# Optimization experiments

Measured on AMD Instinct MI355X. Metric: run time of the kernel, lower is better.

The kernel has to match this reference:

```python
import jax, jax.numpy as jnp
import numpy as np

LAMBDA = 0.5
TAU = 1.0
EPS = 1e-8  # torch F.cosine_similarity eps

B, D = 8192, 1024


def setup_inputs() -> dict:
    key = jax.random.key(0)
    k1, k2, k3, k4 = jax.random.split(key, 4)
    return {
        "student_query_emb": jax.random.normal(k1, (B, D), dtype=jnp.float32),
        "student_passage_emb": jax.random.normal(k2, (B, D), dtype=jnp.float32),
        "teacher_query_emb": jax.random.normal(k3, (B, D), dtype=jnp.float32),
        "teacher_passage_emb": jax.random.normal(k4, (B, D), dtype=jnp.float32),
    }


def _mse(a, b):
    d = a - b
    return jnp.mean(d * d)


def _retrieval_loss(q, p):
    # cosine sim = (q . p) / max(||q|| * ||p||, eps); normalize then matmul
    # (avoids the [B,B,D] broadcast intermediate of the torch version)
    qn = q / jnp.maximum(jnp.linalg.norm(q, axis=-1, keepdims=True), EPS)
    pn = p / jnp.maximum(jnp.linalg.norm(p, axis=-1, keepdims=True), EPS)
    logits = jnp.einsum("bd,cd->bc", qn, pn) / TAU  # [B, B]
    # cross-entropy with labels = arange(B): pick the diagonal log-prob
    logprobs = jax.nn.log_softmax(logits, axis=-1)
    return -jnp.mean(jnp.diagonal(logprobs))


def reference(student_query_emb, student_passage_emb, teacher_query_emb, teacher_passage_emb):
    distill = 0.5 * (_mse(student_query_emb, teacher_query_emb)
                     + _mse(student_passage_emb, teacher_passage_emb))
    retrieval = _retrieval_loss(student_query_emb, student_passage_emb)
    return LAMBDA * distill + (1.0 - LAMBDA) * retrieval
```

## Files before the change

### kernel.cpp

```cpp
#include <hip/hip_runtime.h>
#include <hip/hip_bf16.h>

typedef unsigned short u16;
typedef unsigned char u8;
typedef float f32x4 __attribute__((ext_vector_type(4)));
typedef int int4v __attribute__((ext_vector_type(4)));
typedef int int8v __attribute__((ext_vector_type(8)));

#define B_ROWS 8192
#define D_DIM  1024
#define FP8_SCALE 16.0f
#define ACC_UNSCALE (1.0f/256.0f)


__global__ void __launch_bounds__(256) prep_kernel(
    const float* __restrict__ sq, const float* __restrict__ sp,
    const float* __restrict__ tq, const float* __restrict__ tp,
    int* __restrict__ qn, int* __restrict__ pn,
    float* __restrict__ ppq, float* __restrict__ ppp, float* __restrict__ ppd)
{
    const int wave = threadIdx.x >> 6;
    const int l    = threadIdx.x & 63;
    const int r    = blockIdx.x * 4 + wave;
    const size_t rb4 = (size_t)r * (D_DIM / 4);

    const float4* Q4 = (const float4*)sq + rb4;
    const float4* P4 = (const float4*)sp + rb4;
    const float4* A4 = (const float4*)tq + rb4;
    const float4* B4 = (const float4*)tp + rb4;

    float4 qv[4], pv[4];
    float sq2 = 0.f, sp2 = 0.f, dq = 0.f, dp = 0.f, qp = 0.f;
    #pragma unroll
    for (int j = 0; j < 4; ++j) {
        const int idx = j * 64 + l;
        float4 q = Q4[idx], p = P4[idx], a = A4[idx], b = B4[idx];
        qv[j] = q; pv[j] = p;
        sq2 += q.x*q.x + q.y*q.y + q.z*q.z + q.w*q.w;
        sp2 += p.x*p.x + p.y*p.y + p.z*p.z + p.w*p.w;
        float dx = q.x-a.x, dy = q.y-a.y, dz = q.z-a.z, dw = q.w-a.w;
        dq += dx*dx + dy*dy + dz*dz + dw*dw;
        dx = p.x-b.x; dy = p.y-b.y; dz = p.z-b.z; dw = p.w-b.w;
        dp += dx*dx + dy*dy + dz*dz + dw*dw;
        qp += q.x*p.x + q.y*p.y + q.z*p.z + q.w*p.w;
    }

    #pragma unroll
    for (int m = 1; m <= 32; m <<= 1) {
        sq2 += __shfl_xor(sq2, m);
        sp2 += __shfl_xor(sp2, m);
        dq  += __shfl_xor(dq, m);
        dp  += __shfl_xor(dp, m);
        qp  += __shfl_xor(qp, m);
    }

    const float rq = 1.0f / fmaxf(sqrtf(sq2), 1e-8f);
    const float rp = 1.0f / fmaxf(sqrtf(sp2), 1e-8f);

    if (l == 0) {
        ppq[r] = dq;
        ppp[r] = dp;
        ppd[r] = qp * rq * rp;
    }

    const float fq = rq * FP8_SCALE;
    const float fp = rp * FP8_SCALE;
    int* qrow = qn + (size_t)r * (D_DIM / 4);
    int* prow = pn + (size_t)r * (D_DIM / 4);
    #pragma unroll
    for (int j = 0; j < 4; ++j) {
        const int idx = j * 64 + l;
        int pk = __builtin_amdgcn_cvt_pk_fp8_f32(qv[j].x * fq, qv[j].y * fq, 0, false);
        pk     = __builtin_amdgcn_cvt_pk_fp8_f32(qv[j].z * fq, qv[j].w * fq, pk, true);
        qrow[idx] = pk;
        pk = __builtin_amdgcn_cvt_pk_fp8_f32(pv[j].x * fp, pv[j].y * fp, 0, false);
        pk = __builtin_amdgcn_cvt_pk_fp8_f32(pv[j].z * fp, pv[j].w * fp, pk, true);
        prow[idx] = pk;
    }
}

__global__ void __launch_bounds__(256) gemm_rowsum_kernel(
    const u8* __restrict__ Q, const u8* __restrict__ P,
    float* __restrict__ gpart)
{
    __shared__ u8 smA[128 * 128];
    __shared__ u8 smB[128 * 128];

    const int tid  = threadIdx.x;
    const int wave = tid >> 6;
    const int lane = tid & 63;
    const int bm = blockIdx.y;
    const int bn = blockIdx.x;

    const int lrow   = lane >> 3;
    const int gchunk = (lane & 7) ^ lrow;
    const u8* Ag = Q + ((size_t)bm * 128) * D_DIM + gchunk * 16;
    const u8* Bg = P + ((size_t)bn * 128) * D_DIM + gchunk * 16;

    const int quad  = lane >> 4;
    const int rw    = lane & 15;
    const int r7    = lane & 7;
    const int arow0 = (wave >> 1) * 64;
    const int bcol0 = (wave & 1) * 64;

    const int off_lo = ((2 * quad) ^ r7) * 16;
    const int off_hi = ((2 * quad + 1) ^ r7) * 16;

    f32x4 acc[4][4];
    #pragma unroll
    for (int i = 0; i < 4; ++i)
        #pragma unroll
        for (int j = 0; j < 4; ++j)
            acc[i][j] = (f32x4){0.f, 0.f, 0.f, 0.f};

    for (int k0 = 0; k0 < D_DIM; k0 += 128) {
        #pragma unroll
        for (int i = 0; i < 4; ++i) {
            const int r0 = wave * 32 + i * 8;
            __builtin_amdgcn_global_load_lds(
                (const __attribute__((address_space(1))) void*)(Ag + (size_t)(r0 + lrow) * D_DIM + k0),
                (__attribute__((address_space(3))) void*)(smA + r0 * 128), 16, 0, 0);
            __builtin_amdgcn_global_load_lds(
                (const __attribute__((address_space(1))) void*)(Bg + (size_t)(r0 + lrow) * D_DIM + k0),
                (__attribute__((address_space(3))) void*)(smB + r0 * 128), 16, 0, 0);
        }
        __syncthreads();

        union Frag { int8v v8; struct { int4v lo, hi; } h; };
        Frag af[4], bf[4];
        #pragma unroll
        for (int mi = 0; mi < 4; ++mi)
            af[mi].h.lo = *(const int4v*)(smA + (arow0 + mi * 16 + rw) * 128 + off_lo);
        #pragma unroll
        for (int ni = 0; ni < 4; ++ni)
            bf[ni].h.lo = *(const int4v*)(smB + (bcol0 + ni * 16 + rw) * 128 + off_lo);
        __builtin_amdgcn_sched_barrier(0);
        #pragma unroll
        for (int mi = 0; mi < 4; ++mi)
            af[mi].h.hi = *(const int4v*)(smA + (arow0 + mi * 16 + rw) * 128 + off_hi);
        #pragma unroll
        for (int ni = 0; ni < 4; ++ni)
            bf[ni].h.hi = *(const int4v*)(smB + (bcol0 + ni * 16 + rw) * 128 + off_hi);

        #pragma unroll
        for (int mi = 0; mi < 4; ++mi)
            #pragma unroll
            for (int ni = 0; ni < 4; ++ni)
                acc[mi][ni] = __builtin_amdgcn_mfma_scale_f32_16x16x128_f8f6f4(
                    af[mi].v8, bf[ni].v8, acc[mi][ni],
                    0, 0,
                    0, 0x7f7f7f7f,
                    0, 0x7f7f7f7f);
        __syncthreads();
    }

    float esum[4][4];
    #pragma unroll
    for (int mi = 0; mi < 4; ++mi)
        #pragma unroll
        for (int r = 0; r < 4; ++r) {
            float s = 0.f;
            #pragma unroll
            for (int ni = 0; ni < 4; ++ni)
                s += __expf(acc[mi][ni][r] * ACC_UNSCALE);
            esum[mi][r] = s;
        }
    #pragma unroll
    for (int m = 1; m <= 8; m <<= 1)
        #pragma unroll
        for (int mi = 0; mi < 4; ++mi)
            #pragma unroll
            for (int r = 0; r < 4; ++r)
                esum[mi][r] += __shfl_xor(esum[mi][r], m);

    if (rw == 0) {
        float* dst = gpart + ((size_t)(bn * 2 + (wave & 1))) * B_ROWS
                   + bm * 128 + arow0;
        #pragma unroll
        for (int mi = 0; mi < 4; ++mi)
            #pragma unroll
            for (int r = 0; r < 4; ++r)
                dst[mi * 16 + quad * 4 + r] = esum[mi][r];
    }
}

__global__ void __launch_bounds__(256) reduce_kernel(
    const float* __restrict__ gpart,
    const float* __restrict__ ppq, const float* __restrict__ ppp,
    const float* __restrict__ ppd, float4* __restrict__ bpart)
{
    const int t = threadIdx.x;
    const int r = blockIdx.x * 256 + t;
    float s = 0.f;
    #pragma unroll 8
    for (int j = 0; j < 128; ++j) s += gpart[(size_t)j * B_ROWS + r];
    float ls = logf(s);
    float v2 = ppq[r], v3 = ppp[r], v4 = ppd[r];
    #pragma unroll
    for (int m = 1; m <= 32; m <<= 1) {
        ls += __shfl_xor(ls, m);
        v2 += __shfl_xor(v2, m);
        v3 += __shfl_xor(v3, m);
        v4 += __shfl_xor(v4, m);
    }
    __shared__ float red[4][4];
    if ((t & 63) == 0) {
        red[t >> 6][0] = ls; red[t >> 6][1] = v2;
        red[t >> 6][2] = v3; red[t >> 6][3] = v4;
    }
    __syncthreads();
    if (t == 0) {
        float4 o;
        o.x = red[0][0] + red[1][0] + red[2][0] + red[3][0];
        o.y = red[0][1] + red[1][1] + red[2][1] + red[3][1];
        o.z = red[0][2] + red[1][2] + red[2][2] + red[3][2];
        o.w = red[0][3] + red[1][3] + red[2][3] + red[3][3];
        bpart[blockIdx.x] = o;
    }
}

__global__ void __launch_bounds__(64) finalize_kernel(
    const float4* __restrict__ bpart, float* __restrict__ out)
{
    const int t = threadIdx.x;
    float4 v = (t < 32) ? bpart[t] : (float4){0.f, 0.f, 0.f, 0.f};
    #pragma unroll
    for (int m = 1; m <= 16; m <<= 1) {
        v.x += __shfl_xor(v.x, m);
        v.y += __shfl_xor(v.y, m);
        v.z += __shfl_xor(v.z, m);
        v.w += __shfl_xor(v.w, m);
    }
    if (t == 0) {
        const float inv_bd = 1.0f / ((float)B_ROWS * (float)D_DIM);
        float distill   = 0.5f * (v.y + v.z) * inv_bd;
        float retrieval = (v.x - v.w) / (float)B_ROWS;
        out[0] = 0.5f * distill + 0.5f * retrieval;
    }
}

extern "C" void kernel_launch(void* const* d_in, const int* in_sizes, int n_in,
                              void* d_out, int out_size, void* d_ws, size_t ws_size,
                              hipStream_t stream) {
    const float* sq = (const float*)d_in[0];
    const float* sp = (const float*)d_in[1];
    const float* tq = (const float*)d_in[2];
    const float* tp = (const float*)d_in[3];

    char* ws = (char*)d_ws;
    float*  ppq   = (float*)(ws);
    float*  ppp   = (float*)(ws + 32768);
    float*  ppd   = (float*)(ws + 65536);
    float4* bpart = (float4*)(ws + 98304);
    float*  gpart = (float*)(ws + 131072);
    int*    qn    = (int*)(ws + 131072 + (size_t)128 * B_ROWS * 4);
    int*    pn    = (int*)((char*)qn + (size_t)B_ROWS * D_DIM);

    prep_kernel<<<B_ROWS / 4, 256, 0, stream>>>(sq, sp, tq, tp, qn, pn, ppq, ppp, ppd);
    gemm_rowsum_kernel<<<dim3(64, 64), 256, 0, stream>>>((const u8*)qn, (const u8*)pn, gpart);
    reduce_kernel<<<32, 256, 0, stream>>>(gpart, ppq, ppp, ppd, bpart);
    finalize_kernel<<<1, 64, 0, stream>>>(bpart, (float*)d_out);
}
```

Before: 244.1 us.

## Use two waves per 128x128 tile with 64x128 per-wave subtiles

The GEMM block shrinks from four waves to two, and each wave now computes a 64x128 output subtile (4x8 MFMA accumulators) instead of 64x64. This raises register-level reuse of the A fragments and halves the per-row partial sums written to gpart, so the reduce kernel reads 64 partials instead of 128. The cost is doubled accumulator registers per wave and fewer waves per block to hide LDS and global load latency. B fragments are loaded per column tile, interleaved with the MFMAs.

Measured after the change: 252.2 us. 3.3% more time.

```diff
diff --git a/kernel.cpp b/kernel.cpp
--- a/kernel.cpp
+++ b/kernel.cpp
@@ -79,7 +79,7 @@
     }
 }
 
-__global__ void __launch_bounds__(256) gemm_rowsum_kernel(
+__global__ void __launch_bounds__(128, 2) gemm_rowsum_kernel(
     const u8* __restrict__ Q, const u8* __restrict__ P,
     float* __restrict__ gpart)
 {
@@ -100,23 +100,24 @@
     const int quad  = lane >> 4;
     const int rw    = lane & 15;
     const int r7    = lane & 7;
-    const int arow0 = (wave >> 1) * 64;
-    const int bcol0 = (wave & 1) * 64;
+    const int arow0 = wave * 64;
 
     const int off_lo = ((2 * quad) ^ r7) * 16;
     const int off_hi = ((2 * quad + 1) ^ r7) * 16;
 
-    f32x4 acc[4][4];
+    f32x4 acc[4][8];
     #pragma unroll
     for (int i = 0; i < 4; ++i)
         #pragma unroll
-        for (int j = 0; j < 4; ++j)
+        for (int j = 0; j < 8; ++j)
             acc[i][j] = (f32x4){0.f, 0.f, 0.f, 0.f};
 
+    union Frag { int8v v8; struct { int4v lo, hi; } h; };
+
     for (int k0 = 0; k0 < D_DIM; k0 += 128) {
         #pragma unroll
-        for (int i = 0; i < 4; ++i) {
-            const int r0 = wave * 32 + i * 8;
+        for (int i = 0; i < 8; ++i) {
+            const int r0 = wave * 64 + i * 8;
             __builtin_amdgcn_global_load_lds(
                 (const __attribute__((address_space(1))) void*)(Ag + (size_t)(r0 + lrow) * D_DIM + k0),
                 (__attribute__((address_space(3))) void*)(smA + r0 * 128), 16, 0, 0);
@@ -126,31 +127,27 @@
         }
         __syncthreads();
 
-        union Frag { int8v v8; struct { int4v lo, hi; } h; };
-        Frag af[4], bf[4];
-        #pragma unroll
-        for (int mi = 0; mi < 4; ++mi)
-            af[mi].h.lo = *(const int4v*)(smA + (arow0 + mi * 16 + rw) * 128 + off_lo);
-        #pragma unroll
-        for (int ni = 0; ni < 4; ++ni)
-            bf[ni].h.lo = *(const int4v*)(smB + (bcol0 + ni * 16 + rw) * 128 + off_lo);
-        __builtin_amdgcn_sched_barrier(0);
-        #pragma unroll
-        for (int mi = 0; mi < 4; ++mi)
-            af[mi].h.hi = *(const int4v*)(smA + (arow0 + mi * 16 + rw) * 128 + off_hi);
-        #pragma unroll
-        for (int ni = 0; ni < 4; ++ni)
-            bf[ni].h.hi = *(const int4v*)(smB + (bcol0 + ni * 16 + rw) * 128 + off_hi);
-
-        #pragma unroll
-        for (int mi = 0; mi < 4; ++mi)
-            #pragma unroll
-            for (int ni = 0; ni < 4; ++ni)
+        Frag af[4];
+        #pragma unroll
+        for (int mi = 0; mi < 4; ++mi) {
+            const u8* row = smA + (arow0 + mi * 16 + rw) * 128;
+            af[mi].h.lo = *(const int4v*)(row + off_lo);
+            af[mi].h.hi = *(const int4v*)(row + off_hi);
+        }
+        #pragma unroll
+        for (int ni = 0; ni < 8; ++ni) {
+            Frag bf;
+            const u8* row = smB + (ni * 16 + rw) * 128;
+            bf.h.lo = *(const int4v*)(row + off_lo);
+            bf.h.hi = *(const int4v*)(row + off_hi);
+            #pragma unroll
+            for (int mi = 0; mi < 4; ++mi)
                 acc[mi][ni] = __builtin_amdgcn_mfma_scale_f32_16x16x128_f8f6f4(
-                    af[mi].v8, bf[ni].v8, acc[mi][ni],
+                    af[mi].v8, bf.v8, acc[mi][ni],
                     0, 0,
                     0, 0x7f7f7f7f,
                     0, 0x7f7f7f7f);
+        }
         __syncthreads();
     }
 
@@ -161,7 +158,7 @@
         for (int r = 0; r < 4; ++r) {
             float s = 0.f;
             #pragma unroll
-            for (int ni = 0; ni < 4; ++ni)
+            for (int ni = 0; ni < 8; ++ni)
                 s += __expf(acc[mi][ni][r] * ACC_UNSCALE);
             esum[mi][r] = s;
         }
@@ -174,8 +171,7 @@
                 esum[mi][r] += __shfl_xor(esum[mi][r], m);
 
     if (rw == 0) {
-        float* dst = gpart + ((size_t)(bn * 2 + (wave & 1))) * B_ROWS
-                   + bm * 128 + arow0;
+        float* dst = gpart + (size_t)bn * B_ROWS + bm * 128 + arow0;
         #pragma unroll
         for (int mi = 0; mi < 4; ++mi)
             #pragma unroll
@@ -193,7 +189,7 @@
     const int r = blockIdx.x * 256 + t;
     float s = 0.f;
     #pragma unroll 8
-    for (int j = 0; j < 128; ++j) s += gpart[(size_t)j * B_ROWS + r];
+    for (int j = 0; j < 64; ++j) s += gpart[(size_t)j * B_ROWS + r];
     float ls = logf(s);
     float v2 = ppq[r], v3 = ppp[r], v4 = ppd[r];
     #pragma unroll
@@ -253,11 +249,11 @@
     float*  ppd   = (float*)(ws + 65536);
     float4* bpart = (float4*)(ws + 98304);
     float*  gpart = (float*)(ws + 131072);
-    int*    qn    = (int*)(ws + 131072 + (size_t)128 * B_ROWS * 4);
+    int*    qn    = (int*)(ws + 131072 + (size_t)64 * B_ROWS * 4);
     int*    pn    = (int*)((char*)qn + (size_t)B_ROWS * D_DIM);
 
     prep_kernel<<<B_ROWS / 4, 256, 0, stream>>>(sq, sp, tq, tp, qn, pn, ppq, ppp, ppd);
-    gemm_rowsum_kernel<<<dim3(64, 64), 256, 0, stream>>>((const u8*)qn, (const u8*)pn, gpart);
+    gemm_rowsum_kernel<<<dim3(64, 64), 128, 0, stream>>>((const u8*)qn, (const u8*)pn, gpart);
     reduce_kernel<<<32, 256, 0, stream>>>(gpart, ppq, ppp, ppd, bpart);
     finalize_kernel<<<1, 64, 0, stream>>>(bpart, (float*)d_out);
 }
```

## Fuse prep, GEMM, reduce and finalize into one persistent kernel with grid barriers

Applied to the files above, without the earlier changes.

Replaces the four separate launches with a single persistent kernel of 512 blocks. The blocks step through the prep rows, GEMM tiles and reductions in turn, separated by atomic-counter grid barriers, and the counters are reset with a memset before launch. The aim is to remove the launch gaps and tail effects between stages. In exchange, every block must be co-resident for the barriers to make progress, the GEMM loses the scheduling of a large hardware grid, and an extra memset call is added.

New measurement: 641.3 us. 163% more time.

```diff
diff --git a/kernel.cpp b/kernel.cpp
--- a/kernel.cpp
+++ b/kernel.cpp
@@ -1,7 +1,6 @@
 #include <hip/hip_runtime.h>
 #include <hip/hip_bf16.h>
 
-typedef unsigned short u16;
 typedef unsigned char u8;
 typedef float f32x4 __attribute__((ext_vector_type(4)));
 typedef int int4v __attribute__((ext_vector_type(4)));
@@ -11,231 +10,239 @@
 #define D_DIM  1024
 #define FP8_SCALE 16.0f
 #define ACC_UNSCALE (1.0f/256.0f)
-
-
-__global__ void __launch_bounds__(256) prep_kernel(
+#define NBLK 512
+
+
+__device__ __forceinline__ void grid_barrier(int* ctr) {
+    __syncthreads();
+    if (threadIdx.x == 0) {
+        __threadfence();
+        __hip_atomic_fetch_add(ctr, 1, __ATOMIC_ACQ_REL, __HIP_MEMORY_SCOPE_AGENT);
+        while (__hip_atomic_load(ctr, __ATOMIC_ACQUIRE, __HIP_MEMORY_SCOPE_AGENT) < NBLK)
+            __builtin_amdgcn_s_sleep(2);
+        __threadfence();
+    }
+    __syncthreads();
+}
+
+__global__ void __launch_bounds__(256, 4) mega_kernel(
     const float* __restrict__ sq, const float* __restrict__ sp,
     const float* __restrict__ tq, const float* __restrict__ tp,
     int* __restrict__ qn, int* __restrict__ pn,
-    float* __restrict__ ppq, float* __restrict__ ppp, float* __restrict__ ppd)
-{
-    const int wave = threadIdx.x >> 6;
-    const int l    = threadIdx.x & 63;
-    const int r    = blockIdx.x * 4 + wave;
-    const size_t rb4 = (size_t)r * (D_DIM / 4);
-
-    const float4* Q4 = (const float4*)sq + rb4;
-    const float4* P4 = (const float4*)sp + rb4;
-    const float4* A4 = (const float4*)tq + rb4;
-    const float4* B4 = (const float4*)tp + rb4;
-
-    float4 qv[4], pv[4];
-    float sq2 = 0.f, sp2 = 0.f, dq = 0.f, dp = 0.f, qp = 0.f;
-    #pragma unroll
-    for (int j = 0; j < 4; ++j) {
-        const int idx = j * 64 + l;
-        float4 q = Q4[idx], p = P4[idx], a = A4[idx], b = B4[idx];
-        qv[j] = q; pv[j] = p;
-        sq2 += q.x*q.x + q.y*q.y + q.z*q.z + q.w*q.w;
-        sp2 += p.x*p.x + p.y*p.y + p.z*p.z + p.w*p.w;
-        float dx = q.x-a.x, dy = q.y-a.y, dz = q.z-a.z, dw = q.w-a.w;
-        dq += dx*dx + dy*dy + dz*dz + dw*dw;
-        dx = p.x-b.x; dy = p.y-b.y; dz = p.z-b.z; dw = p.w-b.w;
-        dp += dx*dx + dy*dy + dz*dz + dw*dw;
-        qp += q.x*p.x + q.y*p.y + q.z*p.z + q.w*p.w;
-    }
-
-    #pragma unroll
-    for (int m = 1; m <= 32; m <<= 1) {
-        sq2 += __shfl_xor(sq2, m);
-        sp2 += __shfl_xor(sp2, m);
-        dq  += __shfl_xor(dq, m);
-        dp  += __shfl_xor(dp, m);
-        qp  += __shfl_xor(qp, m);
-    }
-
-    const float rq = 1.0f / fmaxf(sqrtf(sq2), 1e-8f);
-    const float rp = 1.0f / fmaxf(sqrtf(sp2), 1e-8f);
-
-    if (l == 0) {
-        ppq[r] = dq;
-        ppp[r] = dp;
-        ppd[r] = qp * rq * rp;
-    }
-
-    const float fq = rq * FP8_SCALE;
-    const float fp = rp * FP8_SCALE;
-    int* qrow = qn + (size_t)r * (D_DIM / 4);
-    int* prow = pn + (size_t)r * (D_DIM / 4);
-    #pragma unroll
-    for (int j = 0; j < 4; ++j) {
-        const int idx = j * 64 + l;
-        int pk = __builtin_amdgcn_cvt_pk_fp8_f32(qv[j].x * fq, qv[j].y * fq, 0, false);
-        pk     = __builtin_amdgcn_cvt_pk_fp8_f32(qv[j].z * fq, qv[j].w * fq, pk, true);
-        qrow[idx] = pk;
-        pk = __builtin_amdgcn_cvt_pk_fp8_f32(pv[j].x * fp, pv[j].y * fp, 0, false);
-        pk = __builtin_amdgcn_cvt_pk_fp8_f32(pv[j].z * fp, pv[j].w * fp, pk, true);
-        prow[idx] = pk;
-    }
-}
-
-__global__ void __launch_bounds__(256) gemm_rowsum_kernel(
-    const u8* __restrict__ Q, const u8* __restrict__ P,
-    float* __restrict__ gpart)
+    float* __restrict__ ppq, float* __restrict__ ppp, float* __restrict__ ppd,
+    float* __restrict__ gpart, float4* __restrict__ bpart,
+    int* __restrict__ ctrs, float* __restrict__ out)
 {
     __shared__ u8 smA[128 * 128];
     __shared__ u8 smB[128 * 128];
+    __shared__ float red[4][4];
 
     const int tid  = threadIdx.x;
     const int wave = tid >> 6;
     const int lane = tid & 63;
-    const int bm = blockIdx.y;
-    const int bn = blockIdx.x;
-
-    const int lrow   = lane >> 3;
-    const int gchunk = (lane & 7) ^ lrow;
-    const u8* Ag = Q + ((size_t)bm * 128) * D_DIM + gchunk * 16;
-    const u8* Bg = P + ((size_t)bn * 128) * D_DIM + gchunk * 16;
-
-    const int quad  = lane >> 4;
-    const int rw    = lane & 15;
-    const int r7    = lane & 7;
-    const int arow0 = (wave >> 1) * 64;
-    const int bcol0 = (wave & 1) * 64;
-
-    const int off_lo = ((2 * quad) ^ r7) * 16;
-    const int off_hi = ((2 * quad + 1) ^ r7) * 16;
-
-    f32x4 acc[4][4];
-    #pragma unroll
-    for (int i = 0; i < 4; ++i)
-        #pragma unroll
-        for (int j = 0; j < 4; ++j)
-            acc[i][j] = (f32x4){0.f, 0.f, 0.f, 0.f};
-
-    for (int k0 = 0; k0 < D_DIM; k0 += 128) {
-        #pragma unroll
-        for (int i = 0; i < 4; ++i) {
-            const int r0 = wave * 32 + i * 8;
-            __builtin_amdgcn_global_load_lds(
-                (const __attribute__((address_space(1))) void*)(Ag + (size_t)(r0 + lrow) * D_DIM + k0),
-                (__attribute__((address_space(3))) void*)(smA + r0 * 128), 16, 0, 0);
-            __builtin_amdgcn_global_load_lds(
-                (const __attribute__((address_space(1))) void*)(Bg + (size_t)(r0 + lrow) * D_DIM + k0),
-                (__attribute__((address_space(3))) void*)(smB + r0 * 128), 16, 0, 0);
+    const int b    = blockIdx.x;
+
+    #pragma unroll 1
+    for (int i = 0; i < 4; ++i) {
+        const int r = b * 4 + wave + i * 2048;
+        const size_t rb4 = (size_t)r * (D_DIM / 4);
+        const float4* Q4 = (const float4*)sq + rb4;
+        const float4* P4 = (const float4*)sp + rb4;
+        const float4* A4 = (const float4*)tq + rb4;
+        const float4* B4 = (const float4*)tp + rb4;
+
+        float4 qv[4], pv[4];
+        float sq2 = 0.f, sp2 = 0.f, dq = 0.f, dp = 0.f, qp = 0.f;
+        #pragma unroll
+        for (int j = 0; j < 4; ++j) {
+            const int idx = j * 64 + lane;
+            float4 q = Q4[idx], p = P4[idx], a = A4[idx], bb = B4[idx];
+            qv[j] = q; pv[j] = p;
+            sq2 += q.x*q.x + q.y*q.y + q.z*q.z + q.w*q.w;
+            sp2 += p.x*p.x + p.y*p.y + p.z*p.z + p.w*p.w;
+            float dx = q.x-a.x, dy = q.y-a.y, dz = q.z-a.z, dw = q.w-a.w;
+            dq += dx*dx + dy*dy + dz*dz + dw*dw;
+            dx = p.x-bb.x; dy = p.y-bb.y; dz = p.z-bb.z; dw = p.w-bb.w;
+            dp += dx*dx + dy*dy + dz*dz + dw*dw;
+            qp += q.x*p.x + q.y*p.y + q.z*p.z + q.w*p.w;
+        }
+        #pragma unroll
+        for (int m = 1; m <= 32; m <<= 1) {
+            sq2 += __shfl_xor(sq2, m);
+            sp2 += __shfl_xor(sp2, m);
+            dq  += __shfl_xor(dq, m);
+            dp  += __shfl_xor(dp, m);
+            qp  += __shfl_xor(qp, m);
+        }
+        const float rq = 1.0f / fmaxf(sqrtf(sq2), 1e-8f);
+        const float rp = 1.0f / fmaxf(sqrtf(sp2), 1e-8f);
+        if (lane == 0) {
+            ppq[r] = dq;
+            ppp[r] = dp;
+            ppd[r] = qp * rq * rp;
+        }
+        const float fq = rq * FP8_SCALE;
+        const float fp = rp * FP8_SCALE;
+        int* qrow = qn + (size_t)r * (D_DIM / 4);
+        int* prow = pn + (size_t)r * (D_DIM / 4);
+        #pragma unroll
+        for (int j = 0; j < 4; ++j) {
+            const int idx = j * 64 + lane;
+            int pk = __builtin_amdgcn_cvt_pk_fp8_f32(qv[j].x * fq, qv[j].y * fq, 0, false);
+            pk     = __builtin_amdgcn_cvt_pk_fp8_f32(qv[j].z * fq, qv[j].w * fq, pk, true);
+            qrow[idx] = pk;
+            pk = __builtin_amdgcn_cvt_pk_fp8_f32(pv[j].x * fp, pv[j].y * fp, 0, false);
+            pk = __builtin_amdgcn_cvt_pk_fp8_f32(pv[j].z * fp, pv[j].w * fp, pk, true);
+            prow[idx] = pk;
+        }
+    }
+    grid_barrier(&ctrs[0]);
+
+    {
+        const int lrow   = lane >> 3;
+        const int gchunk = (lane & 7) ^ lrow;
+        const int quad   = lane >> 4;
+        const int rw     = lane & 15;
+        const int r7     = lane & 7;
+        const int arow0  = (wave >> 1) * 64;
+        const int bcol0  = (wave & 1) * 64;
+        const int off_lo = ((2 * quad) ^ r7) * 16;
+        const int off_hi = ((2 * quad + 1) ^ r7) * 16;
+
+        union Frag { int8v v8; struct { int4v lo, hi; } h; };
+
+        #pragma unroll 1
+        for (int ti = 0; ti < 8; ++ti) {
+            const int t  = b + ti * NBLK;
+            const int bn = t & 63;
+            const int bm = t >> 6;
+            const u8* Ag = (const u8*)qn + ((size_t)bm * 128) * D_DIM + gchunk * 16;
+            const u8* Bg = (const u8*)pn + ((size_t)bn * 128) * D_DIM + gchunk * 16;
+
+            f32x4 acc[4][4];
+            #pragma unroll
+            for (int i = 0; i < 4; ++i)
+                #pragma unroll
+                for (int j = 0; j < 4; ++j)
+                    acc[i][j] = (f32x4){0.f, 0.f, 0.f, 0.f};
+
+            for (int k0 = 0; k0 < D_DIM; k0 += 128) {
+                #pragma unroll
+                for (int i = 0; i < 4; ++i) {
+                    const int r0 = wave * 32 + i * 8;
+                    __builtin_amdgcn_global_load_lds(
+                        (const __attribute__((address_space(1))) void*)(Ag + (size_t)(r0 + lrow) * D_DIM + k0),
+                        (__attribute__((address_space(3))) void*)(smA + r0 * 128), 16, 0, 0);
+                    __builtin_amdgcn_global_load_lds(
+                        (const __attribute__((address_space(1))) void*)(Bg + (size_t)(r0 + lrow) * D_DIM + k0),
+                        (__attribute__((address_space(3))) void*)(smB + r0 * 128), 16, 0, 0);
+                }
+                __syncthreads();
+
+                Frag af[4], bf[4];
+                #pragma unroll
+                for (int mi = 0; mi < 4; ++mi)
+                    af[mi].h.lo = *(const int4v*)(smA + (arow0 + mi * 16 + rw) * 128 + off_lo);
+                #pragma unroll
+                for (int ni = 0; ni < 4; ++ni)
+                    bf[ni].h.lo = *(const int4v*)(smB + (bcol0 + ni * 16 + rw) * 128 + off_lo);
+                __builtin_amdgcn_sched_barrier(0);
+                #pragma unroll
+                for (int mi = 0; mi < 4; ++mi)
+                    af[mi].h.hi = *(const int4v*)(smA + (arow0 + mi * 16 + rw) * 128 + off_hi);
+                #pragma unroll
+                for (int ni = 0; ni < 4; ++ni)
+                    bf[ni].h.hi = *(const int4v*)(smB + (bcol0 + ni * 16 + rw) * 128 + off_hi);
+
+                #pragma unroll
+                for (int mi = 0; mi < 4; ++mi)
+                    #pragma unroll
+                    for (int ni = 0; ni < 4; ++ni)
+                        acc[mi][ni] = __builtin_amdgcn_mfma_scale_f32_16x16x128_f8f6f4(
+                            af[mi].v8, bf[ni].v8, acc[mi][ni],
+                            0, 0,
+                            0, 0x7f7f7f7f,
+                            0, 0x7f7f7f7f);
+                __syncthreads();
+            }
+
+            float esum[4][4];
+            #pragma unroll
+            for (int mi = 0; mi < 4; ++mi)
+                #pragma unroll
+                for (int r = 0; r < 4; ++r) {
+                    float s = 0.f;
+                    #pragma unroll
+                    for (int ni = 0; ni < 4; ++ni)
+                        s += __expf(acc[mi][ni][r] * ACC_UNSCALE);
+                    esum[mi][r] = s;
+                }
+            #pragma unroll
+            for (int m = 1; m <= 8; m <<= 1)
+                #pragma unroll
+                for (int mi = 0; mi < 4; ++mi)
+                    #pragma unroll
+                    for (int r = 0; r < 4; ++r)
+                        esum[mi][r] += __shfl_xor(esum[mi][r], m);
+
+            if (rw == 0) {
+                float* dst = gpart + ((size_t)(bn * 2 + (wave & 1))) * B_ROWS
+                           + bm * 128 + arow0;
+                #pragma unroll
+                for (int mi = 0; mi < 4; ++mi)
+                    #pragma unroll
+                    for (int r = 0; r < 4; ++r)
+                        dst[mi * 16 + quad * 4 + r] = esum[mi][r];
+            }
+        }
+    }
+    grid_barrier(&ctrs[1]);
+
+    if (b < 32) {
+        const int r = b * 256 + tid;
+        float s = 0.f;
+        #pragma unroll 8
+        for (int j = 0; j < 128; ++j) s += gpart[(size_t)j * B_ROWS + r];
+        float ls = logf(s);
+        float v2 = ppq[r], v3 = ppp[r], v4 = ppd[r];
+        #pragma unroll
+        for (int m = 1; m <= 32; m <<= 1) {
+            ls += __shfl_xor(ls, m);
+            v2 += __shfl_xor(v2, m);
+            v3 += __shfl_xor(v3, m);
+            v4 += __shfl_xor(v4, m);
+        }
+        if (lane == 0) {
+            red[wave][0] = ls; red[wave][1] = v2;
+            red[wave][2] = v3; red[wave][3] = v4;
         }
         __syncthreads();
-
-        union Frag { int8v v8; struct { int4v lo, hi; } h; };
-        Frag af[4], bf[4];
-        #pragma unroll
-        for (int mi = 0; mi < 4; ++mi)
-            af[mi].h.lo = *(const int4v*)(smA + (arow0 + mi * 16 + rw) * 128 + off_lo);
-        #pragma unroll
-        for (int ni = 0; ni < 4; ++ni)
-            bf[ni].h.lo = *(const int4v*)(smB + (bcol0 + ni * 16 + rw) * 128 + off_lo);
-        __builtin_amdgcn_sched_barrier(0);
-        #pragma unroll
-        for (int mi = 0; mi < 4; ++mi)
-            af[mi].h.hi = *(const int4v*)(smA + (arow0 + mi * 16 + rw) * 128 + off_hi);
-        #pragma unroll
-        for (int ni = 0; ni < 4; ++ni)
-            bf[ni].h.hi = *(const int4v*)(smB + (bcol0 + ni * 16 + rw) * 128 + off_hi);
-
-        #pragma unroll
-        for (int mi = 0; mi < 4; ++mi)
-            #pragma unroll
-            for (int ni = 0; ni < 4; ++ni)
-                acc[mi][ni] = __builtin_amdgcn_mfma_scale_f32_16x16x128_f8f6f4(
-                    af[mi].v8, bf[ni].v8, acc[mi][ni],
-                    0, 0,
-                    0, 0x7f7f7f7f,
-                    0, 0x7f7f7f7f);
-        __syncthreads();
-    }
-
-    float esum[4][4];
-    #pragma unroll
-    for (int mi = 0; mi < 4; ++mi)
-        #pragma unroll
-        for (int r = 0; r < 4; ++r) {
-            float s = 0.f;
-            #pragma unroll
-            for (int ni = 0; ni < 4; ++ni)
-                s += __expf(acc[mi][ni][r] * ACC_UNSCALE);
-            esum[mi][r] = s;
-        }
-    #pragma unroll
-    for (int m = 1; m <= 8; m <<= 1)
-        #pragma unroll
-        for (int mi = 0; mi < 4; ++mi)
-            #pragma unroll
-            for (int r = 0; r < 4; ++r)
-                esum[mi][r] += __shfl_xor(esum[mi][r], m);
-
-    if (rw == 0) {
-        float* dst = gpart + ((size_t)(bn * 2 + (wave & 1))) * B_ROWS
-                   + bm * 128 + arow0;
-        #pragma unroll
-        for (int mi = 0; mi < 4; ++mi)
-            #pragma unroll
-            for (int r = 0; r < 4; ++r)
-                dst[mi * 16 + quad * 4 + r] = esum[mi][r];
-    }
-}
-
-__global__ void __launch_bounds__(256) reduce_kernel(
-    const float* __restrict__ gpart,
-    const float* __restrict__ ppq, const float* __restrict__ ppp,
-    const float* __restrict__ ppd, float4* __restrict__ bpart)
-{
-    const int t = threadIdx.x;
-    const int r = blockIdx.x * 256 + t;
-    float s = 0.f;
-    #pragma unroll 8
-    for (int j = 0; j < 128; ++j) s += gpart[(size_t)j * B_ROWS + r];
-    float ls = logf(s);
-    float v2 = ppq[r], v3 = ppp[r], v4 = ppd[r];
-    #pragma unroll
-    for (int m = 1; m <= 32; m <<= 1) {
-        ls += __shfl_xor(ls, m);
-        v2 += __shfl_xor(v2, m);
-        v3 += __shfl_xor(v3, m);
-        v4 += __shfl_xor(v4, m);
-    }
-    __shared__ float red[4][4];
-    if ((t & 63) == 0) {
-        red[t >> 6][0] = ls; red[t >> 6][1] = v2;
-        red[t >> 6][2] = v3; red[t >> 6][3] = v4;
-    }
-    __syncthreads();
-    if (t == 0) {
-        float4 o;
-        o.x = red[0][0] + red[1][0] + red[2][0] + red[3][0];
-        o.y = red[0][1] + red[1][1] + red[2][1] + red[3][1];
-        o.z = red[0][2] + red[1][2] + red[2][2] + red[3][2];
-        o.w = red[0][3] + red[1][3] + red[2][3] + red[3][3];
-        bpart[blockIdx.x] = o;
-    }
-}
-
-__global__ void __launch_bounds__(64) finalize_kernel(
-    const float4* __restrict__ bpart, float* __restrict__ out)
-{
-    const int t = threadIdx.x;
-    float4 v = (t < 32) ? bpart[t] : (float4){0.f, 0.f, 0.f, 0.f};
-    #pragma unroll
-    for (int m = 1; m <= 16; m <<= 1) {
-        v.x += __shfl_xor(v.x, m);
-        v.y += __shfl_xor(v.y, m);
-        v.z += __shfl_xor(v.z, m);
-        v.w += __shfl_xor(v.w, m);
-    }
-    if (t == 0) {
-        const float inv_bd = 1.0f / ((float)B_ROWS * (float)D_DIM);
-        float distill   = 0.5f * (v.y + v.z) * inv_bd;
-        float retrieval = (v.x - v.w) / (float)B_ROWS;
-        out[0] = 0.5f * distill + 0.5f * retrieval;
+        if (tid == 0) {
+            float4 o;
+            o.x = red[0][0] + red[1][0] + red[2][0] + red[3][0];
+            o.y = red[0][1] + red[1][1] + red[2][1] + red[3][1];
+            o.z = red[0][2] + red[1][2] + red[2][2] + red[3][2];
+            o.w = red[0][3] + red[1][3] + red[2][3] + red[3][3];
+            bpart[b] = o;
+        }
+    }
+    grid_barrier(&ctrs[2]);
+
+    if (b == 0 && tid < 32) {
+        float4 v = bpart[tid];
+        #pragma unroll
+        for (int m = 1; m <= 16; m <<= 1) {
+            v.x += __shfl_xor(v.x, m);
+            v.y += __shfl_xor(v.y, m);
+            v.z += __shfl_xor(v.z, m);
+            v.w += __shfl_xor(v.w, m);
+        }
+        if (tid == 0) {
+            const float inv_bd = 1.0f / ((float)B_ROWS * (float)D_DIM);
+            float distill   = 0.5f * (v.y + v.z) * inv_bd;
+            float retrieval = (v.x - v.w) / (float)B_ROWS;
+            out[0] = 0.5f * distill + 0.5f * retrieval;
+        }
     }
 }
 
@@ -252,12 +259,13 @@
     float*  ppp   = (float*)(ws + 32768);
     float*  ppd   = (float*)(ws + 65536);
     float4* bpart = (float4*)(ws + 98304);
+    int*    ctrs  = (int*)(ws + 98816);
     float*  gpart = (float*)(ws + 131072);
     int*    qn    = (int*)(ws + 131072 + (size_t)128 * B_ROWS * 4);
     int*    pn    = (int*)((char*)qn + (size_t)B_ROWS * D_DIM);
 
-    prep_kernel<<<B_ROWS / 4, 256, 0, stream>>>(sq, sp, tq, tp, qn, pn, ppq, ppp, ppd);
-    gemm_rowsum_kernel<<<dim3(64, 64), 256, 0, stream>>>((const u8*)qn, (const u8*)pn, gpart);
-    reduce_kernel<<<32, 256, 0, stream>>>(gpart, ppq, ppp, ppd, bpart);
-    finalize_kernel<<<1, 64, 0, stream>>>(bpart, (float*)d_out);
+    hipMemsetAsync(ctrs, 0, 64, stream);
+    mega_kernel<<<NBLK, 256, 0, stream>>>(sq, sp, tq, tp, qn, pn,
+                                          ppq, ppp, ppd, gpart, bpart,
+                                          ctrs, (float*)d_out);
 }
```
